# Performance work log

Measured on AMD Instinct MI355X. Metric: run time of the kernel, lower is better.

## Reference

```python
import jax, jax.numpy as jnp
import numpy as np

NUM_CLASSES = 20
NUM_ANCHORS = 3
BBOX_ATTRS = 5 + NUM_CLASSES
IMG_H = IMG_W = 416
IN_H = IN_W = 52
CONF_THRES = 0.5
NMS_THRES = 0.4
TOP_K = 2048


def setup_inputs() -> dict:
    key = jax.random.key(0)
    k1, _ = jax.random.split(key)
    inp = jax.random.normal(k1, (16, NUM_ANCHORS * BBOX_ATTRS, IN_H, IN_W), dtype=jnp.float32)
    anchors = jnp.array([[116.0, 90.0], [156.0, 198.0], [373.0, 326.0]], dtype=jnp.float32)
    return {"input": inp, "anchors": anchors}


def decode(inp, anchors):
    """YOLOv3 head decode (YOLOv3Loss.forward with targets=None).
    inp: [B, A*(5+C), H, W] -> output: [B, A*H*W, 5+C] with (cx, cy, w, h, conf, cls...)."""
    bs = inp.shape[0]
    stride_h = IMG_H / IN_H
    stride_w = IMG_W / IN_W
    scaled_anchors = anchors / jnp.array([stride_w, stride_h], dtype=inp.dtype)  # [A, 2]
    # [B, A, H, W, 5+C]
    pred = inp.reshape(bs, NUM_ANCHORS, BBOX_ATTRS, IN_H, IN_W).transpose(0, 1, 3, 4, 2)
    x = jax.nn.sigmoid(pred[..., 0])
    y = jax.nn.sigmoid(pred[..., 1])
    w = pred[..., 2]
    h = pred[..., 3]
    conf = jax.nn.sigmoid(pred[..., 4])
    pred_cls = jax.nn.sigmoid(pred[..., 5:])
    grid_x = jnp.arange(IN_W, dtype=inp.dtype)[None, None, None, :]
    grid_y = jnp.arange(IN_H, dtype=inp.dtype)[None, None, :, None]
    anchor_w = scaled_anchors[:, 0][None, :, None, None]
    anchor_h = scaled_anchors[:, 1][None, :, None, None]
    bx = (x + grid_x) * stride_w
    by = (y + grid_y) * stride_h
    bw = jnp.exp(w) * anchor_w * stride_w
    bh = jnp.exp(h) * anchor_h * stride_h
    boxes = jnp.stack([bx, by, bw, bh], axis=-1).reshape(bs, -1, 4)
    output = jnp.concatenate(
        [boxes, conf.reshape(bs, -1, 1), pred_cls.reshape(bs, -1, NUM_CLASSES)], axis=-1
    )
    return output


def _nms_one(corners, conf, cls_pred):
    """Greedy class-aware NMS over TOP_K conf-sorted candidates.
    corners: [K,4] x1y1x2y2, conf: [K] desc-sorted, cls_pred: [K] int32.
    Returns keep mask [K] bool."""
    x1, y1, x2, y2 = corners[:, 0], corners[:, 1], corners[:, 2], corners[:, 3]
    area = (x2 - x1 + 1.0) * (y2 - y1 + 1.0)
    ix1 = jnp.maximum(x1[:, None], x1[None, :])
    iy1 = jnp.maximum(y1[:, None], y1[None, :])
    ix2 = jnp.minimum(x2[:, None], x2[None, :])
    iy2 = jnp.minimum(y2[:, None], y2[None, :])
    inter = jnp.clip(ix2 - ix1 + 1.0, 0.0) * jnp.clip(iy2 - iy1 + 1.0, 0.0)
    iou = inter / (area[:, None] + area[None, :] - inter + 1e-16)
    # suppress j if kept i (earlier, higher conf, same class) overlaps >= thres
    cond = (iou >= NMS_THRES) & (cls_pred[:, None] == cls_pred[None, :])
    valid = conf >= CONF_THRES
    K = conf.shape[0]
    idx = jnp.arange(K)

    def body(i, carry):
        keep, supp = carry
        ki = valid[i] & (~supp[i])
        keep = keep.at[i].set(ki)
        supp = supp | (cond[i] & (idx > i) & ki)
        return keep, supp

    keep, _ = jax.lax.fori_loop(0, K, body, (jnp.zeros(K, bool), jnp.zeros(K, bool)))
    return keep


def reference(input, anchors):
    output = decode(input, anchors)  # [B, N, 5+C]
    conf = output[..., 4]
    # top-K candidates by objectness (desc order == conf sort in original NMS)
    top_conf, top_idx = jax.lax.top_k(conf, TOP_K)  # [B, K]
    boxes = output[..., :4]
    cx, cy, w, h = boxes[..., 0], boxes[..., 1], boxes[..., 2], boxes[..., 3]
    corners = jnp.stack([cx - w / 2, cy - h / 2, cx + w / 2, cy + h / 2], axis=-1)
    corners_s = jnp.take_along_axis(corners, top_idx[..., None], axis=1)  # [B, K, 4]
    cls_pred = jnp.argmax(output[..., 5:], axis=-1).astype(jnp.int32)  # [B, N]
    cls_s = jnp.take_along_axis(cls_pred, top_idx, axis=1)  # [B, K]
    keep = jax.vmap(_nms_one)(corners_s, top_conf, cls_s)  # [B, K] bool
    return output, top_idx, keep
```

## Files before the change

kernel.cpp:

```cpp
#include <hip/hip_runtime.h>

#pragma clang fp contract(off)

#define B 16
#define A 3
#define HGT 52
#define WID 52
#define HW 2704
#define NCAND 8112
#define CATTR 25
#define TOPK 2048
#define NWORD 64
#define CH 256
#define NCHUNK (TOPK / CH)
#define GPC (CH / 32)
#define CHP 260
#define EPT 8

typedef unsigned int uint32;
typedef unsigned long long u64;

__global__ __launch_bounds__(256) void decode_kernel(const float* __restrict__ inp,
                                                     const float* __restrict__ anchors,
                                                     float* __restrict__ out,
                                                     float* __restrict__ cws,
                                                     float* __restrict__ pk) {
    __shared__ float sm[256 * CATTR];
    int tid = threadIdx.x;
    int t = blockIdx.x * 256 + tid;
    int b  = t / NCAND;
    int n  = t - b * NCAND;
    int a  = n / HW;
    int hw = n - a * HW;
    int gy = hw / WID;
    int gx = hw - gy * WID;
    const float* ip = inp + ((size_t)(b * (A * CATTR) + a * CATTR)) * HW + hw;
    float* sp = sm + tid * CATTR;

    float p0 = ip[0 * HW], p1 = ip[1 * HW], p2 = ip[2 * HW], p3 = ip[3 * HW], p4 = ip[4 * HW];
    float sx = 1.0f / (1.0f + expf(-p0));
    float sy = 1.0f / (1.0f + expf(-p1));
    float bx = (sx + (float)gx) * 8.0f;
    float by = (sy + (float)gy) * 8.0f;
    float bw = expf(p2) * anchors[a * 2 + 0];
    float bh = expf(p3) * anchors[a * 2 + 1];
    float cf = 1.0f / (1.0f + expf(-p4));
    sp[0] = bx; sp[1] = by; sp[2] = bw; sp[3] = bh; sp[4] = cf;
    cws[t] = cf;

    float best = -1.0f; int bc = 0;
#pragma unroll
    for (int c = 0; c < 20; ++c) {
        float v = ip[(5 + c) * HW];
        float s = 1.0f / (1.0f + expf(-v));
        sp[5 + c] = s;
        if (s > best) { best = s; bc = c; }
    }

    float hw_ = bw * 0.5f, hh_ = bh * 0.5f;
    float x1 = bx - hw_, y1 = by - hh_, x2 = bx + hw_, y2 = by + hh_;
    float area = ((x2 - x1) + 1.0f) * ((y2 - y1) + 1.0f);
    float4* pk4 = (float4*)(pk + (size_t)t * 8);
    pk4[0] = make_float4(x1, y1, x2, y2);
    pk4[1] = make_float4(area, (float)bc, (cf >= 0.5f) ? 1.0f : 0.0f, 0.0f);

    __syncthreads();
    const float4* sm4 = (const float4*)sm;
    float4* o4 = (float4*)(out + (size_t)blockIdx.x * 256 * CATTR);
#pragma unroll
    for (int k = 0; k < 6; ++k) o4[k * 256 + tid] = sm4[k * 256 + tid];
    if (tid < 64) o4[1536 + tid] = sm4[1536 + tid];
}

__device__ __forceinline__ void cexd(u64& a, u64& b, bool up) {
    if ((a > b) == up) { u64 tmp = a; a = b; b = tmp; }
}

__device__ __forceinline__ u64 sel(u64 k, u64 o, bool kmin) {
    return kmin ? (k < o ? k : o) : (k > o ? k : o);
}

__global__ __launch_bounds__(256) void sort1_kernel(const float* __restrict__ conf,
                                                    u64* __restrict__ runs) {
    __shared__ u64 mb[2048];
    int blk = blockIdx.x;
    int b = blk >> 2, c = blk & 3;
    int t = threadIdx.x;
    int base = t * EPT;
    int gbase = c * 2048 + base;
    const float* cp = conf + b * NCAND;

    u64 key[EPT];
    if (gbase + EPT <= NCAND) {
        const float4* cp4 = (const float4*)(cp + gbase);
        float4 c0 = cp4[0], c1 = cp4[1];
        float cf[EPT] = {c0.x, c0.y, c0.z, c0.w, c1.x, c1.y, c1.z, c1.w};
#pragma unroll
        for (int e = 0; e < EPT; ++e) {
            unsigned bits = __float_as_uint(cf[e]) | 0x80000000u;
            key[e] = ((u64)(~bits) << 32) | (unsigned)(gbase + e);
        }
    } else {
#pragma unroll
        for (int e = 0; e < EPT; ++e) {
            int idx = gbase + e;
            if (idx < NCAND) {
                unsigned bits = __float_as_uint(cp[idx]) | 0x80000000u;
                key[e] = ((u64)(~bits) << 32) | (unsigned)idx;
            } else key[e] = ~0ull;
        }
    }

    cexd(key[0], key[1], true); cexd(key[2], key[3], false);
    cexd(key[4], key[5], true); cexd(key[6], key[7], false);

    cexd(key[0], key[2], true);  cexd(key[1], key[3], true);
    cexd(key[4], key[6], false); cexd(key[5], key[7], false);
    cexd(key[0], key[1], true);  cexd(key[2], key[3], true);
    cexd(key[4], key[5], false); cexd(key[6], key[7], false);

    bool up8 = ((t & 1) == 0);
    cexd(key[0], key[4], up8); cexd(key[1], key[5], up8);
    cexd(key[2], key[6], up8); cexd(key[3], key[7], up8);
    cexd(key[0], key[2], up8); cexd(key[1], key[3], up8);
    cexd(key[4], key[6], up8); cexd(key[5], key[7], up8);
    cexd(key[0], key[1], up8); cexd(key[2], key[3], up8);
    cexd(key[4], key[5], up8); cexd(key[6], key[7], up8);

    for (unsigned k = 16; k <= 2048; k <<= 1) {
        bool up = (((unsigned)base & k) == 0);
        for (unsigned j = k >> 1; j >= 8; j >>= 1) {
            unsigned m = j >> 3;
            bool kmin = (up == ((t & m) == 0));
            if (m >= 64) {
                __syncthreads();
#pragma unroll
                for (int e = 0; e < EPT; ++e) mb[e * 256 + t] = key[e];
                __syncthreads();
                int pt = t ^ (int)m;
#pragma unroll
                for (int e = 0; e < EPT; ++e) key[e] = sel(key[e], mb[e * 256 + pt], kmin);
            } else {
#pragma unroll
                for (int e = 0; e < EPT; ++e) {
                    u64 o = __shfl_xor(key[e], (int)m);
                    key[e] = sel(key[e], o, kmin);
                }
            }
        }
        cexd(key[0], key[4], up); cexd(key[1], key[5], up);
        cexd(key[2], key[6], up); cexd(key[3], key[7], up);
        cexd(key[0], key[2], up); cexd(key[1], key[3], up);
        cexd(key[4], key[6], up); cexd(key[5], key[7], up);
        cexd(key[0], key[1], up); cexd(key[2], key[3], up);
        cexd(key[4], key[5], up); cexd(key[6], key[7], up);
    }

    u64* R = runs + ((size_t)b * 4 + c) * 2048;
#pragma unroll
    for (int e = 0; e < EPT; ++e) R[base + e] = key[e];
}

__device__ __forceinline__ u64 merge_rank(const u64* __restrict__ Aa,
                                          const u64* __restrict__ Bb, int r) {
    int lo = 0, hi = r;
    while (lo < hi) {
        int mid = (lo + hi) >> 1;
        if (Aa[mid] < Bb[r - 1 - mid]) lo = mid + 1; else hi = mid;
    }
    u64 av = Aa[lo], bv = Bb[r - lo];
    return av < bv ? av : bv;
}

__global__ __launch_bounds__(1024) void topsel_kernel(const u64* __restrict__ runs,
                                                      const float* __restrict__ pk,
                                                      float* __restrict__ topf,
                                                      float* __restrict__ gx1,
                                                      float* __restrict__ gy1,
                                                      float* __restrict__ gx2,
                                                      float* __restrict__ gy2,
                                                      float* __restrict__ gar,
                                                      uint32* __restrict__ gcv,
                                                      uint32* __restrict__ vwords) {
    __shared__ u64 lds[12288];
    int bt  = blockIdx.x;
    int tid = threadIdx.x;
    const u64* R = runs + (size_t)bt * 8192;

#pragma unroll
    for (int k = 0; k < 8; ++k) lds[tid + k * 1024] = R[tid + k * 1024];
    __syncthreads();

    u64* m = lds + 8192;
    u64 v[4];
#pragma unroll
    for (int k = 0; k < 4; ++k) {
        int o = tid + k * 1024;
        int p = o >> 11, r = o & 2047;
        const u64* Aa = lds + p * 4096;
        const u64* Bb = Aa + 2048;
        v[k] = merge_rank(Aa, Bb, r);
    }
#pragma unroll
    for (int k = 0; k < 4; ++k) m[tid + k * 1024] = v[k];
    __syncthreads();

#pragma unroll
    for (int k = 0; k < 2; ++k) {
        int r = tid + k * 1024;
        u64 key = merge_rank(m, m + 2048, r);
        unsigned idx = (unsigned)(key & 0xFFFFFFFFu);
        int t = bt * TOPK + r;
        topf[t] = (float)idx;
        const float4* p4 = (const float4*)(pk + ((size_t)bt * NCAND + idx) * 8);
        float4 g0 = p4[0], g1 = p4[1];
        gx1[t] = g0.x; gy1[t] = g0.y; gx2[t] = g0.z; gy2[t] = g0.w;
        gar[t] = g1.x;
        gcv[t] = (uint32)g1.y;
        bool valid = (g1.z != 0.0f);
        unsigned long long bal = __ballot(valid);
        if ((tid & 63) == 0) {
            vwords[(t >> 5) + 0] = (uint32)bal;
            vwords[(t >> 5) + 1] = (uint32)(bal >> 32);
        }
    }
}

#define KMID (13421772.5 / 33554432.0)
__global__ __launch_bounds__(1024) void build_kernel(const float* __restrict__ gx1,
                                                     const float* __restrict__ gy1,
                                                     const float* __restrict__ gx2,
                                                     const float* __restrict__ gy2,
                                                     const float* __restrict__ gar,
                                                     const uint32* __restrict__ gcv,
                                                     uint32* __restrict__ rowmask) {
    __shared__ float  x1s[TOPK], y1s[TOPK], x2s[TOPK], y2s[TOPK];
    __shared__ uint32 clss[TOPK];
    int bt   = blockIdx.y;
    int pr   = blockIdx.x;
    int tid  = threadIdx.x;
    int lane = tid & 63;
    int wv   = tid >> 6;
    int base = bt * TOPK;
    uint32* rmT = rowmask + (size_t)base * NWORD;

    for (int j = tid; j < TOPK; j += 1024) {
        int g = base + j;
        x1s[j] = gx1[g]; y1s[j] = gy1[g]; x2s[j] = gx2[g]; y2s[j] = gy2[g];
        clss[j] = gcv[g] & 0xffu;
    }
    __syncthreads();

    int r  = (wv >> 3) ? (31 - pr) : pr;
    int i0 = r * 64 + (wv & 7) * 8;

    float rx1[8], ry1[8], rx2[8], ry2[8], rar[8];
    uint32 rcl[8];
#pragma unroll
    for (int k = 0; k < 8; ++k) {
        rx1[k] = x1s[i0 + k]; ry1[k] = y1s[i0 + k];
        rx2[k] = x2s[i0 + k]; ry2[k] = y2s[i0 + k];
        rar[k] = ((rx2[k] - rx1[k]) + 1.0f) * ((ry2[k] - ry1[k]) + 1.0f);
        rcl[k] = clss[i0 + k];
    }

    int j0 = r * 64 + lane;
    float cx1 = x1s[j0], cy1 = y1s[j0], cx2 = x2s[j0], cy2 = y2s[j0];
    uint32 cc = clss[j0];

    for (int cg = r; cg < 32; ++cg) {
        float nx1 = 0.f, ny1 = 0.f, nx2 = 0.f, ny2 = 0.f; uint32 nc = 0;
        if (cg + 1 < 32) {
            int nj = (cg + 1) * 64 + lane;
            nx1 = x1s[nj]; ny1 = y1s[nj]; nx2 = x2s[nj]; ny2 = y2s[nj];
            nc = clss[nj];
        }
        float car = ((cx2 - cx1) + 1.0f) * ((cy2 - cy1) + 1.0f);
        u64 bal[8];
#pragma unroll
        for (int k = 0; k < 8; ++k) {
            float ix1 = fmaxf(rx1[k], cx1);
            float iy1 = fmaxf(ry1[k], cy1);
            float ix2 = fminf(rx2[k], cx2);
            float iy2 = fminf(ry2[k], cy2);
            float iw = fmaxf((ix2 - ix1) + 1.0f, 0.0f);
            float ih = fmaxf((iy2 - iy1) + 1.0f, 0.0f);
            float inter = iw * ih;
            float denom = ((rar[k] + car) - inter) + 1e-16f;
            bool cond = ((double)inter > KMID * (double)denom) && (cc == rcl[k]);
            bal[k] = __ballot(cond);
        }
        u64 v = bal[0];
#pragma unroll
        for (int k = 1; k < 8; ++k) if ((lane & 7) == k) v = bal[k];
        uint32 w32 = (lane & 8) ? (uint32)(v >> 32) : (uint32)v;
        int gi = i0 + (lane & 7);
        int wd = 2 * cg + ((lane >> 3) & 1);
        if (wd == (gi >> 5)) w32 &= ~((2u << (gi & 31)) - 1u);
        if (lane < 16) rmT[(size_t)wd * TOPK + gi] = w32;
        cx1 = nx1; cy1 = ny1; cx2 = nx2; cy2 = ny2; cc = nc;
    }
}

__device__ __forceinline__ void copy_chunk_dma(const uint32* __restrict__ rmT,
                                               uint32* dstL, int c, int wvm1, int lane) {
    int wmin = 8 * c;
    for (int w = wmin + wvm1; w < 64; w += 15) {
        const uint32* gp = rmT + (size_t)w * TOPK + c * CH + lane * 4;
        uint32* lp = dstL + w * CHP;
        __builtin_amdgcn_global_load_lds((const __attribute__((address_space(1))) void*)gp,
                                         (__attribute__((address_space(3))) void*)lp,
                                         16, 0, 0);
    }
}

__global__ __launch_bounds__(1024) void scan_kernel(const uint32* __restrict__ rowmask,
                                                    const uint32* __restrict__ vwords,
                                                    float* __restrict__ keepf) {
    __shared__ uint32 buf[2][64 * CHP];
    int bt  = blockIdx.x;
    int tid = threadIdx.x;
    int wv  = tid >> 6;
    int l   = tid & 63;
    const uint32* rmT = rowmask + (size_t)bt * TOPK * NWORD;

    uint32 supp = 0, keepw = 0;
    if (wv == 0) supp = ~vwords[bt * 64 + l];

    if (wv > 0) copy_chunk_dma(rmT, buf[0], 0, wv - 1, l);
    __syncthreads();

    for (int c = 0; c < NCHUNK; ++c) {
        if (wv > 0) {
            if (c + 1 < NCHUNK) copy_chunk_dma(rmT, buf[(c + 1) & 1], c + 1, wv - 1, l);
        } else {
            const uint32* bp = buf[c & 1];
            uint4 sq[8];
            {
                int g0 = c * GPC;
                const uint4* sp = (const uint4*)(bp + g0 * CHP);
#pragma unroll
                for (int q = 0; q < 8; ++q) sq[q] = sp[q];
            }
            for (int gl = 0; gl < GPC; ++gl) {
                int g = c * GPC + gl;
                uint4 rwq[8];
                const uint4* rp = (const uint4*)(bp + l * CHP + gl * 32);
#pragma unroll
                for (int q = 0; q < 8; ++q) rwq[q] = rp[q];
                uint32 cur = __builtin_amdgcn_readlane(supp, g);
#pragma unroll
                for (int q = 0; q < 8; ++q) {
                    uint32 s0 = sq[q].x, s1 = sq[q].y, s2 = sq[q].z, s3 = sq[q].w;
                    int k = q * 4;
                    cur |= s0 & ((((cur >> (k + 0)) & 1u)) - 1u);
                    cur |= s1 & ((((cur >> (k + 1)) & 1u)) - 1u);
                    cur |= s2 & ((((cur >> (k + 2)) & 1u)) - 1u);
                    cur |= s3 & ((((cur >> (k + 3)) & 1u)) - 1u);
                }
                uint32 keep = ~cur;
                if (l == g) keepw = keep;
                if (gl + 1 < GPC) {
                    const uint4* sp = (const uint4*)(bp + (g + 1) * CHP + (gl + 1) * 32);
#pragma unroll
                    for (int q = 0; q < 8; ++q) sq[q] = sp[q];
                }
                uint32 upd = 0;
#pragma unroll
                for (int q = 0; q < 8; ++q) {
                    int k = q * 4;
                    upd |= rwq[q].x & (uint32)(((int)(keep << (31 - (k + 0)))) >> 31);
                    upd |= rwq[q].y & (uint32)(((int)(keep << (31 - (k + 1)))) >> 31);
                    upd |= rwq[q].z & (uint32)(((int)(keep << (31 - (k + 2)))) >> 31);
                    upd |= rwq[q].w & (uint32)(((int)(keep << (31 - (k + 3)))) >> 31);
                }
                supp |= upd;
            }
        }
        __syncthreads();
    }

    if (wv == 0) {
#pragma unroll
        for (int k = 0; k < 32; ++k)
            keepf[bt * TOPK + l * 32 + k] = (float)((keepw >> k) & 1u);
    }
}

extern "C" void kernel_launch(void* const* d_in, const int* in_sizes, int n_in,
                              void* d_out, int out_size, void* d_ws, size_t ws_size,
                              hipStream_t stream) {
    const float* inp     = (const float*)d_in[0];
    const float* anchors = (const float*)d_in[1];
    float* out   = (float*)d_out;
    float* topf  = out  + (size_t)B * NCAND * CATTR;
    float* keepf = topf + (size_t)B * TOPK;

    float*  cws = (float*)d_ws;
    float*  pk  = cws + B * NCAND;
    float*  gx1 = pk  + (size_t)B * NCAND * 8;
    float*  gy1 = gx1 + B * TOPK;
    float*  gx2 = gy1 + B * TOPK;
    float*  gy2 = gx2 + B * TOPK;
    float*  gar = gy2 + B * TOPK;
    uint32* gcv = (uint32*)(gar + B * TOPK);
    uint32* rowmask = gcv + B * TOPK;
    uint32* vwords  = rowmask + (size_t)B * TOPK * NWORD;
    u64* runs = (u64*)rowmask;

    decode_kernel<<<(B * NCAND) / 256, 256, 0, stream>>>(inp, anchors, out, cws, pk);
    sort1_kernel<<<B * 4, 256, 0, stream>>>(cws, runs);
    topsel_kernel<<<B, 1024, 0, stream>>>(runs, pk, topf, gx1, gy1, gx2, gy2, gar, gcv, vwords);
    build_kernel<<<dim3(16, B), 1024, 0, stream>>>(gx1, gy1, gx2, gy2, gar, gcv, rowmask);
    scan_kernel<<<B, 1024, 0, stream>>>(rowmask, vwords, keepf);
}
```

Measured before the change: 169.4 us.

## Fuse per-chunk bitonic sort and top-K merge into one kernel

Merges sort1 and topsel into a single kernel, one block of 1024 threads per batch. Each group of 256 threads sorts one 2048-element chunk in its own LDS slice, and the block then runs the merge-path selection directly from shared memory. This removes one kernel launch and the global round-trip of the sorted runs. In exchange the sort phase runs on only 16 blocks instead of 64, and the __syncthreads calls inside the sort now synchronise all four groups together.

```diff
diff --git a/kernel.cpp b/kernel.cpp
--- a/kernel.cpp
+++ b/kernel.cpp
@@ -80,15 +80,36 @@
     return kmin ? (k < o ? k : o) : (k > o ? k : o);
 }
 
-__global__ __launch_bounds__(256) void sort1_kernel(const float* __restrict__ conf,
-                                                    u64* __restrict__ runs) {
-    __shared__ u64 mb[2048];
-    int blk = blockIdx.x;
-    int b = blk >> 2, c = blk & 3;
-    int t = threadIdx.x;
-    int base = t * EPT;
-    int gbase = c * 2048 + base;
-    const float* cp = conf + b * NCAND;
+__device__ __forceinline__ u64 merge_rank(const u64* __restrict__ Aa,
+                                          const u64* __restrict__ Bb, int r) {
+    int lo = 0, hi = r;
+    while (lo < hi) {
+        int mid = (lo + hi) >> 1;
+        if (Aa[mid] < Bb[r - 1 - mid]) lo = mid + 1; else hi = mid;
+    }
+    u64 av = Aa[lo], bv = Bb[r - lo];
+    return av < bv ? av : bv;
+}
+
+__global__ __launch_bounds__(1024) void sortsel_kernel(const float* __restrict__ conf,
+                                                       const float* __restrict__ pk,
+                                                       float* __restrict__ topf,
+                                                       float* __restrict__ gx1,
+                                                       float* __restrict__ gy1,
+                                                       float* __restrict__ gx2,
+                                                       float* __restrict__ gy2,
+                                                       float* __restrict__ gar,
+                                                       uint32* __restrict__ gcv,
+                                                       uint32* __restrict__ vwords) {
+    __shared__ u64 smem[12288];
+    int bt  = blockIdx.x;
+    int tid = threadIdx.x;
+    int g   = tid >> 8;
+    int t   = tid & 255;
+    int base  = t * EPT;
+    int gbase = g * 2048 + base;
+    const float* cp = conf + bt * NCAND;
+    u64* mb = smem + g * 2048;
 
     u64 key[EPT];
     if (gbase + EPT <= NCAND) {
@@ -131,7 +152,7 @@
         bool up = (((unsigned)base & k) == 0);
         for (unsigned j = k >> 1; j >= 8; j >>= 1) {
             unsigned m = j >> 3;
-            bool kmin = (up == ((t & m) == 0));
+            bool kmin = (up == ((t & (int)m) == 0));
             if (m >= 64) {
                 __syncthreads();
 #pragma unroll
@@ -156,72 +177,42 @@
         cexd(key[4], key[5], up); cexd(key[6], key[7], up);
     }
 
-    u64* R = runs + ((size_t)b * 4 + c) * 2048;
-#pragma unroll
-    for (int e = 0; e < EPT; ++e) R[base + e] = key[e];
-}
-
-__device__ __forceinline__ u64 merge_rank(const u64* __restrict__ Aa,
-                                          const u64* __restrict__ Bb, int r) {
-    int lo = 0, hi = r;
-    while (lo < hi) {
-        int mid = (lo + hi) >> 1;
-        if (Aa[mid] < Bb[r - 1 - mid]) lo = mid + 1; else hi = mid;
-    }
-    u64 av = Aa[lo], bv = Bb[r - lo];
-    return av < bv ? av : bv;
-}
-
-__global__ __launch_bounds__(1024) void topsel_kernel(const u64* __restrict__ runs,
-                                                      const float* __restrict__ pk,
-                                                      float* __restrict__ topf,
-                                                      float* __restrict__ gx1,
-                                                      float* __restrict__ gy1,
-                                                      float* __restrict__ gx2,
-                                                      float* __restrict__ gy2,
-                                                      float* __restrict__ gar,
-                                                      uint32* __restrict__ gcv,
-                                                      uint32* __restrict__ vwords) {
-    __shared__ u64 lds[12288];
-    int bt  = blockIdx.x;
-    int tid = threadIdx.x;
-    const u64* R = runs + (size_t)bt * 8192;
-
-#pragma unroll
-    for (int k = 0; k < 8; ++k) lds[tid + k * 1024] = R[tid + k * 1024];
-    __syncthreads();
-
-    u64* m = lds + 8192;
+    __syncthreads();
+#pragma unroll
+    for (int e = 0; e < EPT; ++e) mb[base + e] = key[e];
+    __syncthreads();
+
+    u64* m = smem + 8192;
     u64 v[4];
 #pragma unroll
-    for (int k = 0; k < 4; ++k) {
-        int o = tid + k * 1024;
+    for (int k2 = 0; k2 < 4; ++k2) {
+        int o = tid + k2 * 1024;
         int p = o >> 11, r = o & 2047;
-        const u64* Aa = lds + p * 4096;
+        const u64* Aa = smem + p * 4096;
         const u64* Bb = Aa + 2048;
-        v[k] = merge_rank(Aa, Bb, r);
-    }
-#pragma unroll
-    for (int k = 0; k < 4; ++k) m[tid + k * 1024] = v[k];
-    __syncthreads();
-
-#pragma unroll
-    for (int k = 0; k < 2; ++k) {
-        int r = tid + k * 1024;
-        u64 key = merge_rank(m, m + 2048, r);
-        unsigned idx = (unsigned)(key & 0xFFFFFFFFu);
-        int t = bt * TOPK + r;
-        topf[t] = (float)idx;
+        v[k2] = merge_rank(Aa, Bb, r);
+    }
+#pragma unroll
+    for (int k2 = 0; k2 < 4; ++k2) m[tid + k2 * 1024] = v[k2];
+    __syncthreads();
+
+#pragma unroll
+    for (int k2 = 0; k2 < 2; ++k2) {
+        int r = tid + k2 * 1024;
+        u64 kk = merge_rank(m, m + 2048, r);
+        unsigned idx = (unsigned)(kk & 0xFFFFFFFFu);
+        int to = bt * TOPK + r;
+        topf[to] = (float)idx;
         const float4* p4 = (const float4*)(pk + ((size_t)bt * NCAND + idx) * 8);
         float4 g0 = p4[0], g1 = p4[1];
-        gx1[t] = g0.x; gy1[t] = g0.y; gx2[t] = g0.z; gy2[t] = g0.w;
-        gar[t] = g1.x;
-        gcv[t] = (uint32)g1.y;
+        gx1[to] = g0.x; gy1[to] = g0.y; gx2[to] = g0.z; gy2[to] = g0.w;
+        gar[to] = g1.x;
+        gcv[to] = (uint32)g1.y;
         bool valid = (g1.z != 0.0f);
         unsigned long long bal = __ballot(valid);
         if ((tid & 63) == 0) {
-            vwords[(t >> 5) + 0] = (uint32)bal;
-            vwords[(t >> 5) + 1] = (uint32)(bal >> 32);
+            vwords[(to >> 5) + 0] = (uint32)bal;
+            vwords[(to >> 5) + 1] = (uint32)(bal >> 32);
         }
     }
 }
@@ -406,11 +397,9 @@
     uint32* gcv = (uint32*)(gar + B * TOPK);
     uint32* rowmask = gcv + B * TOPK;
     uint32* vwords  = rowmask + (size_t)B * TOPK * NWORD;
-    u64* runs = (u64*)rowmask;
 
     decode_kernel<<<(B * NCAND) / 256, 256, 0, stream>>>(inp, anchors, out, cws, pk);
-    sort1_kernel<<<B * 4, 256, 0, stream>>>(cws, runs);
-    topsel_kernel<<<B, 1024, 0, stream>>>(runs, pk, topf, gx1, gy1, gx2, gy2, gar, gcv, vwords);
+    sortsel_kernel<<<B, 1024, 0, stream>>>(cws, pk, topf, gx1, gy1, gx2, gy2, gar, gcv, vwords);
     build_kernel<<<dim3(16, B), 1024, 0, stream>>>(gx1, gy1, gx2, gy2, gar, gcv, rowmask);
     scan_kernel<<<B, 1024, 0, stream>>>(rowmask, vwords, keepf);
 }
```

Result: slower. 180.7 us (+6.7%).
